# Optimization experiments

Measured on AMD Instinct MI355X. Metric: run time of the kernel, lower is better.

## Reference

```python
import jax, jax.numpy as jnp
import numpy as np

NUM_HEADS = 16
D_MODEL = 1024
HEAD_DIM = D_MODEL // NUM_HEADS  # 64
NEG_INF = -1e9


def alibi_bidirectional_bias(num_heads, seq_len, dtype=jnp.float32):
    """[num_heads, S, S] bias: first H/2 heads forward-causal ALiBi, last H/2 backward."""
    half = num_heads // 2
    base = 24.0 ** (1.0 / half)
    slopes = (1.0 / base ** jnp.arange(1, half + 1, dtype=dtype))[:, None, None]  # [half,1,1]
    pos = jnp.arange(seq_len)
    rel = (pos[None, :] - pos[:, None]).astype(dtype)  # rel[i,j] = j - i
    neg = jnp.full((seq_len, seq_len), NEG_INF, dtype=dtype)
    fwd = slopes * jnp.tril(rel) + jnp.triu(neg, 1)          # causal (attend past)
    bwd = slopes * jnp.triu(-rel) + jnp.tril(neg, -1)        # anti-causal (attend future)
    return jnp.concatenate([fwd, bwd], axis=0)  # [H, S, S]


def setup_inputs() -> dict:
    key = jax.random.key(0)
    ks = jax.random.split(key, 9)
    B, S, D = 2, 2048, D_MODEL
    sc = 1.0 / np.sqrt(D)
    inp = {"x": jax.random.normal(ks[0], (B, S, D), dtype=jnp.float32)}
    inp["Wq"] = jax.random.normal(ks[1], (D, D), dtype=jnp.float32) * sc
    inp["bq"] = jnp.zeros((D,), dtype=jnp.float32)
    inp["Wk"] = jax.random.normal(ks[2], (D, D), dtype=jnp.float32) * sc
    inp["bk"] = jnp.zeros((D,), dtype=jnp.float32)
    inp["Wv"] = jax.random.normal(ks[3], (D, D), dtype=jnp.float32) * sc
    inp["bv"] = jnp.zeros((D,), dtype=jnp.float32)
    inp["Wf"] = jax.random.normal(ks[4], (D, D), dtype=jnp.float32) * sc
    inp["bf"] = jnp.zeros((D,), dtype=jnp.float32)
    return inp


def reference(x, Wq, bq, Wk, bk, Wv, bv, Wf, bf):
    B, S, D = x.shape
    H, hd = NUM_HEADS, HEAD_DIM

    def heads(y):  # [B,S,D] -> [B,H,S,hd]
        return y.reshape(B, S, H, hd).transpose(0, 2, 1, 3)

    q = heads(x @ Wq + bq)
    k = heads(x @ Wk + bk)
    v = heads(x @ Wv + bv)

    bias = alibi_bidirectional_bias(H, S, x.dtype)  # [H,S,S]
    scores = jnp.einsum("bhqd,bhkd->bhqk", q, k) * (1.0 / np.sqrt(hd)) + bias[None]
    attn = jax.nn.softmax(scores, axis=-1)
    out = jnp.einsum("bhqk,bhkd->bhqd", attn, v)
    out = out.transpose(0, 2, 1, 3).reshape(B, S, D)
    return out @ Wf + bf
```

## Files before the change

kernel.cpp:

```cpp
#include <hip/hip_runtime.h>

#define S_LEN 2048
#define NH 16
#define HD 64
#define DM 1024
#define BSZ 2

typedef __bf16 bf16;
typedef __bf16 bf16x8 __attribute__((ext_vector_type(8)));
typedef float f32x4 __attribute__((ext_vector_type(4)));
typedef const unsigned int __attribute__((address_space(1)))* gas_ptr;
typedef unsigned int __attribute__((address_space(3)))* las_ptr;

__device__ __forceinline__ void gl_lds16(const bf16* g, bf16* l) {
  __builtin_amdgcn_global_load_lds((gas_ptr)g, (las_ptr)l, 16, 0, 0);
}

#define CFENCE asm volatile("" ::: "memory")

__global__ __launch_bounds__(256) void k_prep(
    const float* __restrict__ x, bf16* __restrict__ xb,
    const float* __restrict__ W0, const float* __restrict__ W1,
    const float* __restrict__ W2, const float* __restrict__ W3,
    bf16* __restrict__ dqkv, bf16* __restrict__ df) {
  __shared__ float t[64][65];
  const int id = blockIdx.x;
  if (id < 4096) {
    int i = id * 256 + threadIdx.x;
    float4 v = ((const float4*)x)[i];
    union { ushort4 u; bf16 b[4]; } o;
    o.b[0] = (bf16)v.x; o.b[1] = (bf16)v.y; o.b[2] = (bf16)v.z; o.b[3] = (bf16)v.w;
    ((ushort4*)xb)[i] = o.u;
    return;
  }
  const int id2 = id - 4096;
  const int z = id2 >> 8;
  const float* W = (z == 0) ? W0 : (z == 1) ? W1 : (z == 2) ? W2 : W3;
  bf16* D = (z < 3) ? (dqkv + (size_t)z * 1048576) : df;
  int k0 = ((id2 >> 4) & 15) * 64, n0 = (id2 & 15) * 64;
  int c = threadIdx.x & 63, rr = threadIdx.x >> 6;
#pragma unroll
  for (int it = 0; it < 16; ++it) {
    int r = it * 4 + rr;
    t[r][c] = W[(size_t)(k0 + r) * DM + n0 + c];
  }
  __syncthreads();
#pragma unroll
  for (int it = 0; it < 16; ++it) {
    int r = it * 4 + rr;
    D[(size_t)(n0 + r) * DM + k0 + c] = (bf16)t[c][r];
  }
}

template <int MODE, int BM, int BN>
__global__ __launch_bounds__(256) void k_gemm(
    const bf16* __restrict__ A, const bf16* __restrict__ Bt,
    const float* __restrict__ b0, const float* __restrict__ b1,
    const float* __restrict__ b2, void* __restrict__ Cout,
    bf16* __restrict__ VtOut, int M, int N, int K) {
  constexpr int NST = BM / 32 + BN / 32;
  __shared__ __align__(16) bf16 SA[2][BM * 64];
  __shared__ __align__(16) bf16 SB[2][BN * 64];
  constexpr int MIc = BM / 32, NIc = BN / 32;
  const int tid = threadIdx.x;
  const int l = tid & 63, w = tid >> 6;
  const int lm = l & 15, lg = l >> 4;
  const int id = blockIdx.x;
  const int xcd = id & 7, r2 = id >> 3;
  int bx, by;
  if (MODE == 0) {
    bx = (xcd & 3) * 8 + (r2 & 7);
    by = (xcd >> 2) * 12 + (r2 >> 3);
  } else {
    bx = (xcd & 3) * 16 + (r2 & 15);
    by = (xcd >> 2) * 4 + (r2 >> 4);
  }
  const int bm = bx * BM, bn = by * BN;
  const int wm = (w >> 1) * (BM / 2), wn = (w & 1) * (BN / 2);

  f32x4 acc[MIc][NIc] = {};
  const bf16* Ag = A + (size_t)bm * K;
  const bf16* Bg = Bt + (size_t)bn * K;

  auto stage = [&](int k0, int bufi) {
#pragma unroll
    for (int it = 0; it < BM / 32; ++it) {
      int cl = it * 256 + tid;
      int row = cl >> 3;
      int cs = ((cl & 7) ^ (row & 7)) << 3;
      gl_lds16(Ag + (size_t)row * K + k0 + cs, &SA[bufi][(it * 256 + w * 64) * 8]);
    }
#pragma unroll
    for (int it = 0; it < BN / 32; ++it) {
      int cl = it * 256 + tid;
      int row = cl >> 3;
      int cs = ((cl & 7) ^ (row & 7)) << 3;
      gl_lds16(Bg + (size_t)row * K + k0 + cs, &SB[bufi][(it * 256 + w * 64) * 8]);
    }
  };

  stage(0, 0);
  const int nk = K >> 6;
  int buf = 0;
  for (int t = 0; t < nk; ++t) {
    if (t + 1 < nk) {
      stage((t + 1) << 6, buf ^ 1);
      if constexpr (NST == 8) {
        asm volatile("s_waitcnt vmcnt(8)" ::: "memory");
      } else {
        asm volatile("s_waitcnt vmcnt(6)" ::: "memory");
      }
    } else {
      asm volatile("s_waitcnt vmcnt(0)" ::: "memory");
    }
    __builtin_amdgcn_s_barrier();
    CFENCE;
    const bf16* As = SA[buf];
    const bf16* Bs = SB[buf];
#pragma unroll
    for (int kk = 0; kk < 2; ++kk) {
      bf16x8 af[MIc], bfr[NIc];
#pragma unroll
      for (int mi = 0; mi < MIc; ++mi) {
        int row = wm + mi * 16 + lm;
        af[mi] = *(const bf16x8*)&As[row * 64 + ((((kk << 2) + lg) ^ (row & 7)) << 3)];
      }
#pragma unroll
      for (int ni = 0; ni < NIc; ++ni) {
        int row = wn + ni * 16 + lm;
        bfr[ni] = *(const bf16x8*)&Bs[row * 64 + ((((kk << 2) + lg) ^ (row & 7)) << 3)];
      }
#pragma unroll
      for (int mi = 0; mi < MIc; ++mi)
#pragma unroll
        for (int ni = 0; ni < NIc; ++ni)
          acc[mi][ni] = __builtin_amdgcn_mfma_f32_16x16x32_bf16(
              af[mi], bfr[ni], acc[mi][ni], 0, 0, 0);
    }
    CFENCE;
    __builtin_amdgcn_s_barrier();
    CFENCE;
    buf ^= 1;
  }

  if (MODE == 0 && bn >= 2048) {
    bf16* sc = (bf16*)SA;
#pragma unroll
    for (int ni = 0; ni < NIc; ++ni) {
      int n_l = wn + ni * 16 + lm;
      float bv = b2[(bn + n_l) & 1023];
#pragma unroll
      for (int mi = 0; mi < MIc; ++mi) {
        int g = ((wm + mi * 16) >> 2) + lg;
        int gp = g ^ ((n_l & 7) << 2);
        union { ushort4 u; bf16 bb[4]; } pkv;
#pragma unroll
        for (int r = 0; r < 4; ++r) pkv.bb[r] = (bf16)(acc[mi][ni][r] + bv);
        *(ushort4*)&sc[n_l * 128 + gp * 4] = pkv.u;
      }
    }
    __syncthreads();
    const int bq = bm >> 11, s0 = bm & 2047;
#pragma unroll
    for (int it2 = 0; it2 < 8; ++it2) {
      int row = it2 * 16 + (tid >> 4), c = tid & 15;
      int g0p = (2 * c) ^ ((row & 7) << 2);
      float4 val = *(const float4*)&sc[row * 128 + g0p * 4];
      int ng = bn + row;
      int hV = (ng >> 6) & 15;
      int d = ng & 63;
      *(float4*)&VtOut[((size_t)(bq * NH + hV) * HD + d) * S_LEN + s0 + c * 8] = val;
    }
    return;
  }

#pragma unroll
  for (int ni = 0; ni < NIc; ++ni) {
    int n = bn + wn + ni * 16 + lm;
    float bv;
    if (MODE == 0) {
      bv = (n < 1024) ? b0[n] : b1[n & 1023];
    } else {
      bv = b0[n];
    }
#pragma unroll
    for (int mi = 0; mi < MIc; ++mi) {
#pragma unroll
      for (int r = 0; r < 4; ++r) {
        int m = bm + wm + mi * 16 + lg * 4 + r;
        float v = acc[mi][ni][r] + bv;
        if (MODE == 0) {
          int qkv = n >> 10;
          int h = (n >> 6) & 15;
          int d = n & 63;
          int b = m >> 11, s = m & 2047;
          ((bf16*)Cout)[(size_t)qkv * (BSZ * NH * S_LEN * HD) +
                        ((size_t)(b * NH + h) * S_LEN + s) * HD + d] = (bf16)v;
        } else {
          ((float*)Cout)[(size_t)m * N + n] = v;
        }
      }
    }
  }
}

#define SMX(MASKED)                                                           \
  {                                                                           \
    const float t0 = slp2 * (float)dlo;                                       \
    _Pragma("unroll") for (int ni = 0; ni < 4; ++ni) {                        \
      const int koff = (ni & 1) * 32 + (ni >> 1) * 4;                         \
      float bni = t0 + dni[ni];                                               \
      float pr[4];                                                            \
      _Pragma("unroll") for (int r = 0; r < 4; ++r) {                         \
        float v = fmaf(sc[ni][r], c1, bni + srr[r]);                          \
        if (MASKED) {                                                         \
          int reli = dlo + koff + relc + r;                                   \
          bool ok = causal ? (reli <= 0) : (reli >= 0);                       \
          v = ok ? v : -1e9f;                                                 \
        }                                                                     \
        pr[r] = __builtin_amdgcn_exp2f(v);                                    \
      }                                                                       \
      union { bf16 b[2]; unsigned u; } u0, u1;                                \
      u0.b[0] = (bf16)pr[0]; u0.b[1] = (bf16)pr[1];                           \
      u1.b[0] = (bf16)pr[2]; u1.b[1] = (bf16)pr[3];                           \
      pk[ni][0] = u0.u; pk[ni][1] = u1.u;                                     \
    }                                                                         \
  }

__global__ __launch_bounds__(512, 2) void k_attn(const bf16* __restrict__ Qh,
                                                 const bf16* __restrict__ Kh,
                                                 const bf16* __restrict__ Vt,
                                                 bf16* __restrict__ O) {
  __shared__ __align__(16) bf16 Ks[2][4096];
  __shared__ __align__(16) bf16 Vs[2][4096];
  const int id = blockIdx.x;
  const int lam = id >> 3;
  const int bh = ((id & 7) << 2) | (lam & 3);
  const int rho = (lam < 32) ? (lam >> 2) : 15 - ((lam - 32) >> 2);
  const int b = bh >> 4, h = bh & 15;
  const bool causal = (h < 8);
  const int yi = causal ? (15 - rho) : rho;
  const int tid = threadIdx.x;
  const int w = tid >> 6, l = tid & 63;
  const int lm = l & 15, lg = l >> 4;
  const int hh = causal ? h : h - 8;
  const float c1 = 0.18033688f;
  const float sm = __builtin_amdgcn_exp2f(-(float)(hh + 1) * 0.57312035f) * 1.44269504f;
  const float slp2 = causal ? sm : -sm;
  const int relc = lg * 8 - lm;
  const int krow_lane = ((lm >> 2) << 3) + (lm & 3);
  const int swzK = (lm & 3) | (((lm >> 2) & 1) << 2);
  const int swzV = (lm & 3) | (((lm >> 3) & 1) << 2);
  float dni[4], srr[4];
#pragma unroll
  for (int ni = 0; ni < 4; ++ni)
    dni[ni] = slp2 * (float)((ni & 1) * 32 + (ni >> 1) * 4);
#pragma unroll
  for (int r = 0; r < 4; ++r) srr[r] = slp2 * (float)(relc + r);

  const bf16* Qp = Qh + (size_t)bh * S_LEN * HD;
  const bf16* Kp = Kh + (size_t)bh * S_LEN * HD;
  const bf16* Vp = Vt + (size_t)bh * HD * S_LEN;

  bf16x8 ones;
#pragma unroll
  for (int i = 0; i < 8; ++i) ones[i] = (bf16)1.0f;

  auto stage = [&](bf16* lk, bf16* lv, int j0) {
    const int row = tid >> 3, c = tid & 7;
    const int sw = (row & 3) | (((row >> 3) & 1) << 2);
    const int gc = (c ^ sw) << 3;
    const int clb8 = ((tid >> 6) << 6) * 8;
    gl_lds16(Kp + (size_t)(j0 + row) * HD + gc, lk + clb8);
    gl_lds16(Vp + (size_t)row * S_LEN + j0 + gc, lv + clb8);
  };

  const int qb = yi << 7;
  const int q0 = qb + w * 16;
  const int jbase = causal ? 0 : qb;
  const int jcnt = causal ? (qb >> 6) + 2 : ((S_LEN - qb) >> 6);

  bf16x8 qf[2];
#pragma unroll
  for (int kk = 0; kk < 2; ++kk)
    qf[kk] = *(const bf16x8*)&Qp[(size_t)(q0 + lm) * HD + kk * 32 + lg * 8];

  f32x4 oacc[4] = {};
  f32x4 lacc = {};

  auto compute = [&](int t, const bf16* lk, const bf16* lv) {
    const int j0 = jbase + t * 64;
    const int dlo = j0 - q0;
    const bool skip = causal ? (dlo >= 16) : (dlo <= -64);
    if (skip) return;
    f32x4 sc[4] = {};
#pragma unroll
    for (int kk = 0; kk < 2; ++kk)
#pragma unroll
      for (int ni = 0; ni < 4; ++ni) {
        const int koff = (ni & 1) * 32 + (ni >> 1) * 4;
        bf16x8 kf = *(const bf16x8*)&lk[(koff + krow_lane) * 64 +
                                        ((((kk << 2) + lg) ^ swzK) << 3)];
        sc[ni] = __builtin_amdgcn_mfma_f32_16x16x32_bf16(kf, qf[kk], sc[ni],
                                                         0, 0, 0);
      }
    bf16x8 vf[2][4];
#pragma unroll
    for (int kk = 0; kk < 2; ++kk)
#pragma unroll
      for (int di = 0; di < 4; ++di)
        vf[kk][di] = *(const bf16x8*)&lv[(di * 16 + lm) * 64 +
                                         ((((kk << 2) + lg) ^ swzV) << 3)];
    const bool full = causal ? (dlo <= -63) : (dlo >= 15);
    unsigned pk[4][2];
    if (full) { SMX(false); } else { SMX(true); }
#pragma unroll
    for (int kk = 0; kk < 2; ++kk) {
      union { unsigned d[4]; bf16x8 v; } pa;
      pa.d[0] = pk[kk][0];
      pa.d[1] = pk[kk][1];
      pa.d[2] = pk[kk + 2][0];
      pa.d[3] = pk[kk + 2][1];
      lacc = __builtin_amdgcn_mfma_f32_16x16x32_bf16(pa.v, ones, lacc, 0, 0, 0);
#pragma unroll
      for (int di = 0; di < 4; ++di)
        oacc[di] = __builtin_amdgcn_mfma_f32_16x16x32_bf16(pa.v, vf[kk][di],
                                                           oacc[di], 0, 0, 0);
    }
  };

  stage(Ks[0], Vs[0], jbase);
  __syncthreads();
  for (int t = 0; t < jcnt; ++t) {
    const int cur = t & 1;
    if (t + 1 < jcnt) stage(Ks[cur ^ 1], Vs[cur ^ 1], jbase + (t + 1) * 64);
    compute(t, Ks[cur], Vs[cur]);
    __syncthreads();
  }

  float rin[4];
#pragma unroll
  for (int r = 0; r < 4; ++r) rin[r] = 1.0f / lacc[r];
#pragma unroll
  for (int di = 0; di < 4; ++di) {
    int d = h * HD + di * 16 + lm;
#pragma unroll
    for (int r = 0; r < 4; ++r) {
      int q = q0 + lg * 4 + r;
      O[((size_t)b * S_LEN + q) * DM + d] = (bf16)(oacc[di][r] * rin[r]);
    }
  }
}

extern "C" void kernel_launch(void* const* d_in, const int* in_sizes, int n_in,
                              void* d_out, int out_size, void* d_ws, size_t ws_size,
                              hipStream_t stream) {
  const float* x  = (const float*)d_in[0];
  const float* Wq = (const float*)d_in[1];
  const float* bq = (const float*)d_in[2];
  const float* Wk = (const float*)d_in[3];
  const float* bk = (const float*)d_in[4];
  const float* Wv = (const float*)d_in[5];
  const float* bv = (const float*)d_in[6];
  const float* Wf = (const float*)d_in[7];
  const float* bfp = (const float*)d_in[8];

  char* ws = (char*)d_ws;
  const size_t MB = 1ull << 20;
  bf16* xb    = (bf16*)(ws);
  bf16* Wqkvt = (bf16*)(ws + 8 * MB);
  bf16* Wft   = (bf16*)(ws + 14 * MB);
  bf16* QKVh  = (bf16*)(ws + 16 * MB);
  bf16* Vt    = (bf16*)(ws + 40 * MB);
  bf16* O     = QKVh + 2 * 4194304;

  k_prep<<<5120, 256, 0, stream>>>(x, xb, Wq, Wk, Wv, Wf, Wqkvt, Wft);
  k_gemm<0, 128, 128><<<768, 256, 0, stream>>>(
      xb, Wqkvt, bq, bk, bv, QKVh, Vt, 4096, 3072, 1024);
  k_attn<<<512, 512, 0, stream>>>(QKVh, QKVh + 4194304, Vt, O);
  k_gemm<2, 64, 128><<<512, 256, 0, stream>>>(
      O, Wft, bfp, bfp, bfp, d_out, nullptr, 4096, 1024, 1024);
}
```

Baseline: 183.2 us.

## Double attention K/V tile to 128 keys per stage to halve barriers

```diff
diff --git a/kernel.cpp b/kernel.cpp
--- a/kernel.cpp
+++ b/kernel.cpp
@@ -231,8 +231,8 @@
                                                  const bf16* __restrict__ Kh,
                                                  const bf16* __restrict__ Vt,
                                                  bf16* __restrict__ O) {
-  __shared__ __align__(16) bf16 Ks[2][4096];
-  __shared__ __align__(16) bf16 Vs[2][4096];
+  __shared__ __align__(16) bf16 Ks[2][8192];
+  __shared__ __align__(16) bf16 Vs[2][8192];
   const int id = blockIdx.x;
   const int lam = id >> 3;
   const int bh = ((id & 7) << 2) | (lam & 3);
@@ -250,7 +250,6 @@
   const int relc = lg * 8 - lm;
   const int krow_lane = ((lm >> 2) << 3) + (lm & 3);
   const int swzK = (lm & 3) | (((lm >> 2) & 1) << 2);
-  const int swzV = (lm & 3) | (((lm >> 3) & 1) << 2);
   float dni[4], srr[4];
 #pragma unroll
   for (int ni = 0; ni < 4; ++ni)
@@ -267,18 +266,23 @@
   for (int i = 0; i < 8; ++i) ones[i] = (bf16)1.0f;
 
   auto stage = [&](bf16* lk, bf16* lv, int j0) {
-    const int row = tid >> 3, c = tid & 7;
-    const int sw = (row & 3) | (((row >> 3) & 1) << 2);
-    const int gc = (c ^ sw) << 3;
-    const int clb8 = ((tid >> 6) << 6) * 8;
-    gl_lds16(Kp + (size_t)(j0 + row) * HD + gc, lk + clb8);
-    gl_lds16(Vp + (size_t)row * S_LEN + j0 + gc, lv + clb8);
+#pragma unroll
+    for (int it = 0; it < 2; ++it) {
+      const int cl = it * 512 + tid;
+      const int base8 = (it * 512 + w * 64) * 8;
+      const int rowK = cl >> 3, cK = cl & 7;
+      const int swK = (rowK & 3) | (((rowK >> 3) & 1) << 2);
+      gl_lds16(Kp + (size_t)(j0 + rowK) * HD + ((cK ^ swK) << 3), lk + base8);
+      const int rowV = cl >> 4, cV = cl & 15;
+      gl_lds16(Vp + (size_t)rowV * S_LEN + j0 + ((cV ^ (rowV & 7)) << 3),
+               lv + base8);
+    }
   };
 
   const int qb = yi << 7;
   const int q0 = qb + w * 16;
   const int jbase = causal ? 0 : qb;
-  const int jcnt = causal ? (qb >> 6) + 2 : ((S_LEN - qb) >> 6);
+  const int jcnt = causal ? yi + 1 : (16 - yi);
 
   bf16x8 qf[2];
 #pragma unroll
@@ -288,9 +292,8 @@
   f32x4 oacc[4] = {};
   f32x4 lacc = {};
 
-  auto compute = [&](int t, const bf16* lk, const bf16* lv) {
-    const int j0 = jbase + t * 64;
-    const int dlo = j0 - q0;
+  auto compute = [&](int j0h, int half, const bf16* lk, const bf16* lv) {
+    const int dlo = j0h - q0;
     const bool skip = causal ? (dlo >= 16) : (dlo <= -64);
     if (skip) return;
     f32x4 sc[4] = {};
@@ -299,7 +302,7 @@
 #pragma unroll
       for (int ni = 0; ni < 4; ++ni) {
         const int koff = (ni & 1) * 32 + (ni >> 1) * 4;
-        bf16x8 kf = *(const bf16x8*)&lk[(koff + krow_lane) * 64 +
+        bf16x8 kf = *(const bf16x8*)&lk[(half * 64 + koff + krow_lane) * 64 +
                                         ((((kk << 2) + lg) ^ swzK) << 3)];
         sc[ni] = __builtin_amdgcn_mfma_f32_16x16x32_bf16(kf, qf[kk], sc[ni],
                                                          0, 0, 0);
@@ -309,8 +312,8 @@
     for (int kk = 0; kk < 2; ++kk)
 #pragma unroll
       for (int di = 0; di < 4; ++di)
-        vf[kk][di] = *(const bf16x8*)&lv[(di * 16 + lm) * 64 +
-                                         ((((kk << 2) + lg) ^ swzV) << 3)];
+        vf[kk][di] = *(const bf16x8*)&lv[(di * 16 + lm) * 128 +
+                                         ((((half << 3) + (kk << 2) + lg) ^ (lm & 7)) << 3)];
     const bool full = causal ? (dlo <= -63) : (dlo >= 15);
     unsigned pk[4][2];
     if (full) { SMX(false); } else { SMX(true); }
@@ -333,8 +336,10 @@
   __syncthreads();
   for (int t = 0; t < jcnt; ++t) {
     const int cur = t & 1;
-    if (t + 1 < jcnt) stage(Ks[cur ^ 1], Vs[cur ^ 1], jbase + (t + 1) * 64);
-    compute(t, Ks[cur], Vs[cur]);
+    if (t + 1 < jcnt) stage(Ks[cur ^ 1], Vs[cur ^ 1], jbase + (t + 1) * 128);
+    const int j0 = jbase + t * 128;
+    compute(j0, 0, Ks[cur], Vs[cur]);
+    compute(j0 + 64, 1, Ks[cur], Vs[cur]);
     __syncthreads();
   }
 
```

Measured after the change: 191.4 us. 1.05x slower.
